# Kernel tuning notes

Hardware: AMD Instinct MI355X
Metric: run time of the kernel (lower is better)

The kernel has to match this reference:

```python
import jax, jax.numpy as jnp
import numpy as np

N = 50000      # nodes
D = 64         # hidden
EMB = 16       # emb_dims
E = 800000     # edges = N * knn(16)
R2 = 0.3 ** 2  # r^2 at epoch 0
GW = 1.0       # grav_weight at epoch 0
EPS = 1e-5


def _lin_params(k, fi, fo):
    kw, kb = jax.random.split(k)
    W = jax.random.normal(kw, (fi, fo), jnp.float32) / np.sqrt(fi).astype(np.float32)
    b = jax.random.normal(kb, (fo,), jnp.float32) * 0.01
    return W, b


def setup_inputs() -> dict:
    key = jax.random.key(0)
    ks = jax.random.split(key, 16)
    inp = {}
    inp['hidden_features'] = jax.random.normal(ks[0], (N, D), jnp.float32)
    inp['edge_index'] = jax.random.randint(ks[1], (2, E), 0, N, jnp.int32)
    inp['current_epoch'] = 0
    # spatial network: (D+1)->D->D->EMB, each Linear + LayerNorm + ReLU
    for i, (fi, fo) in enumerate([(D + 1, D), (D, D), (D, EMB)]):
        W, b = _lin_params(ks[2 + i], fi, fo)
        inp[f'sW{i}'] = W
        inp[f'sb{i}'] = b
        inp[f'sg{i}'] = jnp.ones((fo,), jnp.float32)
        inp[f'sB{i}'] = jnp.zeros((fo,), jnp.float32)
    # feature network: 2*(D+1)->D->D, each Linear + LayerNorm + ReLU
    for i, (fi, fo) in enumerate([(2 * (D + 1), D), (D, D)]):
        W, b = _lin_params(ks[8 + i], fi, fo)
        inp[f'fW{i}'] = W
        inp[f'fb{i}'] = b
        inp[f'fg{i}'] = jnp.ones((fo,), jnp.float32)
        inp[f'fB{i}'] = jnp.zeros((fo,), jnp.float32)
    return inp


def _ln(x, g, b):
    m = jnp.mean(x, axis=-1, keepdims=True)
    v = jnp.mean((x - m) ** 2, axis=-1, keepdims=True)
    return (x - m) * jax.lax.rsqrt(v + EPS) * g + b


def _blk(x, W, b, g, B):
    return jax.nn.relu(_ln(x @ W + b, g, B))


def reference(hidden_features, edge_index, current_epoch,
              sW0, sb0, sg0, sB0, sW1, sb1, sg1, sB1, sW2, sb2, sg2, sB2,
              fW0, fb0, fg0, fB0, fW1, fb1, fg1, fB1):
    # append per-node mean channel: [N, D] -> [N, D+1]
    h = jnp.concatenate([hidden_features,
                         jnp.mean(hidden_features, axis=1, keepdims=True)], axis=-1)
    # spatial embedding [N, EMB]
    s = _blk(_blk(_blk(h, sW0, sb0, sg0, sB0), sW1, sb1, sg1, sB1), sW2, sb2, sg2, sB2)
    start = edge_index[0]
    end = edge_index[1]
    # gravitational edge weight: exp(-grav_weight * ||s_i - s_j||^2 / r^2)
    d = jnp.sum((s[start] - s[end]) ** 2, axis=-1)  # [E]
    w = jnp.exp(-GW * d / R2)                        # [E]
    # gather -> weight -> scatter_add aggregation
    agg = jax.ops.segment_sum(h[start] * w[:, None], end, num_segments=h.shape[0])
    cat = jnp.concatenate([agg, h], axis=-1)  # [N, 2*(D+1)]
    out = _blk(_blk(cat, fW0, fb0, fg0, fB0), fW1, fb1, fg1, fB1)  # [N, D]
    return out, s
```

## Files before the change

kernel.cpp:

```cpp
#include <hip/hip_runtime.h>
#include <hip/hip_bf16.h>

#define NN 50000
#define DD 64
#define EMBD 16
#define EE 800000
#define CAP 64
#define TILES ((NN + 63) / 64)
#define AGGB ((NN + 3) / 4)

#define OW_S0 0
#define OW_S1 6656
#define OW_S2 11264
#define OW_F0 12416
#define OW_F1 23168
#define NWB   27776

typedef short s16x8 __attribute__((ext_vector_type(8)));
typedef float f32x4 __attribute__((ext_vector_type(4)));
typedef unsigned short ushort_t;

__device__ __forceinline__ float bcast(float v, int l) {
  return __int_as_float(__builtin_amdgcn_readlane(__float_as_int(v), l));
}

__device__ __forceinline__ unsigned short f2b(float x) {
  unsigned u = __float_as_uint(x);
  return (unsigned short)((u + 0x7FFFu + ((u >> 16) & 1u)) >> 16);
}

__device__ __forceinline__ float b2f(unsigned short u) {
  return __uint_as_float(((unsigned)u) << 16);
}

__device__ __forceinline__ float wred64f(float v) {
  v += __shfl_xor(v, 1);  v += __shfl_xor(v, 2);  v += __shfl_xor(v, 4);
  v += __shfl_xor(v, 8);  v += __shfl_xor(v, 16); v += __shfl_xor(v, 32);
  return v;
}

__global__ __launch_bounds__(256)
void GravConv3556_prep_k(const float* __restrict__ sW0, const float* __restrict__ sW1,
                         const float* __restrict__ sW2, const float* __restrict__ fW0,
                         const float* __restrict__ fW1, unsigned short* __restrict__ wb,
                         int* __restrict__ cnt)
{
  int i0 = blockIdx.x * 256 + threadIdx.x;
  int st = gridDim.x * 256;
  for (int i = i0; i < NN; i += st) cnt[i] = 0;
  for (int i = i0; i < 64 * 104; i += st) {
    int n = i / 104, k = i % 104;
    wb[OW_S0 + i] = (k < 65) ? f2b(sW0[k * 64 + n]) : (unsigned short)0;
  }
  for (int i = i0; i < 64 * 72; i += st) {
    int n = i / 72, k = i % 72;
    wb[OW_S1 + i] = (k < 64) ? f2b(sW1[k * 64 + n]) : (unsigned short)0;
  }
  for (int i = i0; i < 16 * 72; i += st) {
    int n = i / 72, k = i % 72;
    wb[OW_S2 + i] = (k < 64) ? f2b(sW2[k * 16 + n]) : (unsigned short)0;
  }
  for (int i = i0; i < 64 * 168; i += st) {
    int n = i / 168, k = i % 168;
    wb[OW_F0 + i] = (k < 130) ? f2b(fW0[k * 64 + n]) : (unsigned short)0;
  }
  for (int i = i0; i < 64 * 72; i += st) {
    int n = i / 72, k = i % 72;
    wb[OW_F1 + i] = (k < 64) ? f2b(fW1[k * 64 + n]) : (unsigned short)0;
  }
}

#define XROW 104
__global__ __launch_bounds__(256)
void GravConv3556_spatial_k(const float* __restrict__ hidden,
    const unsigned short* __restrict__ wb,
    const float* __restrict__ sb0, const float* __restrict__ sg0, const float* __restrict__ sB0,
    const float* __restrict__ sb1, const float* __restrict__ sg1, const float* __restrict__ sB1,
    const float* __restrict__ sb2, const float* __restrict__ sg2, const float* __restrict__ sB2,
    float* __restrict__ s_out)
{
  __shared__ unsigned short X[64 * XROW];
  __shared__ unsigned short W0[64 * XROW];
  __shared__ unsigned short W1[64 * 72];
  __shared__ unsigned short W2[16 * 72];
  int tid = threadIdx.x;
  int lane = tid & 63;
  int wv = tid >> 6;
  int c = lane & 15;
  int q = lane >> 4;
  int base = blockIdx.x * 64;

  {
    const uint4* g = (const uint4*)(wb + OW_S0); uint4* l = (uint4*)W0;
    for (int i = tid; i < 832; i += 256) l[i] = g[i];
    g = (const uint4*)(wb + OW_S1); l = (uint4*)W1;
    for (int i = tid; i < 576; i += 256) l[i] = g[i];
    g = (const uint4*)(wb + OW_S2); l = (uint4*)W2;
    for (int i = tid; i < 144; i += 256) l[i] = g[i];
  }
  for (int i = 0; i < 16; i++) {
    int m = wv * 16 + i;
    int node = base + m; if (node >= NN) node = NN - 1;
    float x = hidden[(size_t)node * 64 + lane];
    float mean = wred64f(x) * (1.0f / 64.0f);
    X[m * XROW + lane] = f2b(x);
    if (lane == 0) X[m * XROW + 64] = f2b(mean);
    if (lane < 39) X[m * XROW + 65 + lane] = 0;
  }
  __syncthreads();

  int mrow = wv * 16 + c;
  float z[16];

  {
    s16x8 a[3];
    #pragma unroll
    for (int kc = 0; kc < 3; kc++)
      a[kc] = *(const s16x8*)(X + mrow * XROW + kc * 32 + q * 8);
    #pragma unroll
    for (int nt = 0; nt < 4; nt++) {
      f32x4 acc = {0.f, 0.f, 0.f, 0.f};
      #pragma unroll
      for (int kc = 0; kc < 3; kc++) {
        s16x8 b = *(const s16x8*)(W0 + (nt * 16 + c) * XROW + kc * 32 + q * 8);
        acc = __builtin_amdgcn_mfma_f32_16x16x32_bf16(a[kc], b, acc, 0, 0, 0);
      }
      float bias = sb0[nt * 16 + c];
      #pragma unroll
      for (int reg = 0; reg < 4; reg++) z[nt * 4 + reg] = acc[reg] + bias;
    }
    #pragma unroll
    for (int reg = 0; reg < 4; reg++) {
      float s1 = z[reg] + z[4 + reg] + z[8 + reg] + z[12 + reg];
      float s2 = z[reg] * z[reg] + z[4 + reg] * z[4 + reg]
               + z[8 + reg] * z[8 + reg] + z[12 + reg] * z[12 + reg];
      s1 += __shfl_xor(s1, 1); s2 += __shfl_xor(s2, 1);
      s1 += __shfl_xor(s1, 2); s2 += __shfl_xor(s2, 2);
      s1 += __shfl_xor(s1, 4); s2 += __shfl_xor(s2, 4);
      s1 += __shfl_xor(s1, 8); s2 += __shfl_xor(s2, 8);
      float mu = s1 * (1.0f / 64.0f);
      float rs = rsqrtf(fmaxf(s2 * (1.0f / 64.0f) - mu * mu, 0.f) + 1e-5f);
      int m = wv * 16 + q * 4 + reg;
      #pragma unroll
      for (int nt = 0; nt < 4; nt++) {
        int n = nt * 16 + c;
        float y = fmaxf(fmaf((z[nt * 4 + reg] - mu) * rs, sg0[n], sB0[n]), 0.f);
        X[m * XROW + n] = f2b(y);
      }
    }
  }

  {
    s16x8 a[2];
    #pragma unroll
    for (int kc = 0; kc < 2; kc++)
      a[kc] = *(const s16x8*)(X + mrow * XROW + kc * 32 + q * 8);
    #pragma unroll
    for (int nt = 0; nt < 4; nt++) {
      f32x4 acc = {0.f, 0.f, 0.f, 0.f};
      #pragma unroll
      for (int kc = 0; kc < 2; kc++) {
        s16x8 b = *(const s16x8*)(W1 + (nt * 16 + c) * 72 + kc * 32 + q * 8);
        acc = __builtin_amdgcn_mfma_f32_16x16x32_bf16(a[kc], b, acc, 0, 0, 0);
      }
      float bias = sb1[nt * 16 + c];
      #pragma unroll
      for (int reg = 0; reg < 4; reg++) z[nt * 4 + reg] = acc[reg] + bias;
    }
    #pragma unroll
    for (int reg = 0; reg < 4; reg++) {
      float s1 = z[reg] + z[4 + reg] + z[8 + reg] + z[12 + reg];
      float s2 = z[reg] * z[reg] + z[4 + reg] * z[4 + reg]
               + z[8 + reg] * z[8 + reg] + z[12 + reg] * z[12 + reg];
      s1 += __shfl_xor(s1, 1); s2 += __shfl_xor(s2, 1);
      s1 += __shfl_xor(s1, 2); s2 += __shfl_xor(s2, 2);
      s1 += __shfl_xor(s1, 4); s2 += __shfl_xor(s2, 4);
      s1 += __shfl_xor(s1, 8); s2 += __shfl_xor(s2, 8);
      float mu = s1 * (1.0f / 64.0f);
      float rs = rsqrtf(fmaxf(s2 * (1.0f / 64.0f) - mu * mu, 0.f) + 1e-5f);
      int m = wv * 16 + q * 4 + reg;
      #pragma unroll
      for (int nt = 0; nt < 4; nt++) {
        int n = nt * 16 + c;
        float y = fmaxf(fmaf((z[nt * 4 + reg] - mu) * rs, sg1[n], sB1[n]), 0.f);
        X[m * XROW + n] = f2b(y);
      }
    }
  }

  {
    s16x8 a[2];
    #pragma unroll
    for (int kc = 0; kc < 2; kc++)
      a[kc] = *(const s16x8*)(X + mrow * XROW + kc * 32 + q * 8);
    f32x4 acc = {0.f, 0.f, 0.f, 0.f};
    #pragma unroll
    for (int kc = 0; kc < 2; kc++) {
      s16x8 b = *(const s16x8*)(W2 + c * 72 + kc * 32 + q * 8);
      acc = __builtin_amdgcn_mfma_f32_16x16x32_bf16(a[kc], b, acc, 0, 0, 0);
    }
    float bias = sb2[c];
    float z4[4];
    #pragma unroll
    for (int reg = 0; reg < 4; reg++) z4[reg] = acc[reg] + bias;
    #pragma unroll
    for (int reg = 0; reg < 4; reg++) {
      float s1 = z4[reg], s2 = z4[reg] * z4[reg];
      s1 += __shfl_xor(s1, 1); s2 += __shfl_xor(s2, 1);
      s1 += __shfl_xor(s1, 2); s2 += __shfl_xor(s2, 2);
      s1 += __shfl_xor(s1, 4); s2 += __shfl_xor(s2, 4);
      s1 += __shfl_xor(s1, 8); s2 += __shfl_xor(s2, 8);
      float mu = s1 * (1.0f / 16.0f);
      float rs = rsqrtf(fmaxf(s2 * (1.0f / 16.0f) - mu * mu, 0.f) + 1e-5f);
      float y = fmaxf(fmaf((z4[reg] - mu) * rs, sg2[c], sB2[c]), 0.f);
      int node = base + wv * 16 + q * 4 + reg;
      if (node < NN) s_out[(size_t)node * 16 + c] = y;
    }
  }
}

__global__ __launch_bounds__(256)
void GravConv3556_scatter_k(const int* __restrict__ ei, const float* __restrict__ s,
                            int* __restrict__ cnt, int2* __restrict__ pairs)
{
  int e = blockIdx.x * 256 + threadIdx.x;
  if (e >= EE) return;
  int a = ei[e];
  int b = ei[EE + e];
  const float4* sa = (const float4*)(s + (size_t)a * 16);
  const float4* sb = (const float4*)(s + (size_t)b * 16);
  float4 p0 = sa[0], p1 = sa[1], p2 = sa[2], p3 = sa[3];
  float4 q0 = sb[0], q1 = sb[1], q2 = sb[2], q3 = sb[3];
  float d = 0.f;
  d = fmaf(p0.x - q0.x, p0.x - q0.x, d); d = fmaf(p0.y - q0.y, p0.y - q0.y, d);
  d = fmaf(p0.z - q0.z, p0.z - q0.z, d); d = fmaf(p0.w - q0.w, p0.w - q0.w, d);
  d = fmaf(p1.x - q1.x, p1.x - q1.x, d); d = fmaf(p1.y - q1.y, p1.y - q1.y, d);
  d = fmaf(p1.z - q1.z, p1.z - q1.z, d); d = fmaf(p1.w - q1.w, p1.w - q1.w, d);
  d = fmaf(p2.x - q2.x, p2.x - q2.x, d); d = fmaf(p2.y - q2.y, p2.y - q2.y, d);
  d = fmaf(p2.z - q2.z, p2.z - q2.z, d); d = fmaf(p2.w - q2.w, p2.w - q2.w, d);
  d = fmaf(p3.x - q3.x, p3.x - q3.x, d); d = fmaf(p3.y - q3.y, p3.y - q3.y, d);
  d = fmaf(p3.z - q3.z, p3.z - q3.z, d); d = fmaf(p3.w - q3.w, p3.w - q3.w, d);
  float w = __expf(d * (-1.0f / 0.09f));
  int pos = atomicAdd(&cnt[b], 1);
  if (pos < CAP) pairs[(size_t)b * CAP + pos] = make_int2(a, __float_as_int(w));
}

__global__ __launch_bounds__(256)
void GravConv3556_agg_k(const float* __restrict__ hidden,
                        const int* __restrict__ cnt, const int2* __restrict__ pairs,
                        unsigned short* __restrict__ aggr)
{
  int lane = threadIdx.x & 63;
  int n = blockIdx.x * 4 + (threadIdx.x >> 6);
  if (n >= NN) return;
  int m = cnt[n]; if (m > CAP) m = CAP;
  float xa0 = 0.f, xa1 = 0.f, xa2 = 0.f, xa3 = 0.f;
  int2 pr = make_int2(0, 0);
  if (lane < m) pr = pairs[(size_t)n * CAP + lane];
  int aj = pr.x; float wj = __int_as_float(pr.y);
#define GSTEP(q, ACC) { int jj = jb + (q); int jc = jj < m ? jj : m - 1;        \
    int   a_ = __builtin_amdgcn_readlane(aj, jc);                               \
    float w_ = (jj < m) ? bcast(wj, jc) : 0.0f;                                 \
    ACC = fmaf(w_, hidden[(size_t)a_ * 64 + lane], ACC); }
  for (int jb = 0; jb < m; jb += 8) {
    GSTEP(0, xa0) GSTEP(1, xa1) GSTEP(2, xa2) GSTEP(3, xa3)
    GSTEP(4, xa0) GSTEP(5, xa1) GSTEP(6, xa2) GSTEP(7, xa3)
  }
#undef GSTEP
  aggr[(size_t)n * 64 + lane] = f2b((xa0 + xa1) + (xa2 + xa3));
}

#define CROW 168
__global__ __launch_bounds__(256)
void GravConv3556_feature_k(const float* __restrict__ hidden,
    const unsigned short* __restrict__ aggr, const unsigned short* __restrict__ wb,
    const float* __restrict__ fb0, const float* __restrict__ fg0, const float* __restrict__ fB0,
    const float* __restrict__ fb1, const float* __restrict__ fg1, const float* __restrict__ fB1,
    float* __restrict__ out)
{
  __shared__ unsigned short catB[64 * CROW];
  __shared__ unsigned short W0T[64 * CROW];
  __shared__ unsigned short W1T[64 * 72];
  int tid = threadIdx.x;
  int lane = tid & 63;
  int wv = tid >> 6;
  int c = lane & 15;
  int q = lane >> 4;
  int base = blockIdx.x * 64;

  {
    const uint4* g = (const uint4*)(wb + OW_F0); uint4* l = (uint4*)W0T;
    for (int i = tid; i < 1344; i += 256) l[i] = g[i];
    g = (const uint4*)(wb + OW_F1); l = (uint4*)W1T;
    for (int i = tid; i < 576; i += 256) l[i] = g[i];
  }

  for (int i = 0; i < 16; i++) {
    int m = wv * 16 + i;
    int node = base + m; if (node >= NN) node = NN - 1;
    unsigned short ra = aggr[(size_t)node * 64 + lane];
    float xa = b2f(ra);
    float mA = wred64f(xa) * (1.0f / 64.0f);
    catB[m * CROW + lane] = ra;
    float xh = hidden[(size_t)node * 64 + lane];
    float mB = wred64f(xh) * (1.0f / 64.0f);
    catB[m * CROW + 65 + lane] = f2b(xh);
    if (lane == 0) {
      catB[m * CROW + 64] = f2b(mA);
      catB[m * CROW + 129] = f2b(mB);
    }
    if (lane < 38) catB[m * CROW + 130 + lane] = 0;
  }
  __syncthreads();

  int mrow = wv * 16 + c;

  s16x8 a0[5];
  #pragma unroll
  for (int kc = 0; kc < 5; kc++)
    a0[kc] = *(const s16x8*)(catB + mrow * CROW + kc * 32 + q * 8);

  float z[16];
  #pragma unroll
  for (int nt = 0; nt < 4; nt++) {
    f32x4 acc = {0.f, 0.f, 0.f, 0.f};
    #pragma unroll
    for (int kc = 0; kc < 5; kc++) {
      s16x8 b = *(const s16x8*)(W0T + (nt * 16 + c) * CROW + kc * 32 + q * 8);
      acc = __builtin_amdgcn_mfma_f32_16x16x32_bf16(a0[kc], b, acc, 0, 0, 0);
    }
    float bias = fb0[nt * 16 + c];
    #pragma unroll
    for (int reg = 0; reg < 4; reg++) z[nt * 4 + reg] = acc[reg] + bias;
  }
  #pragma unroll
  for (int reg = 0; reg < 4; reg++) {
    float s1 = z[reg] + z[4 + reg] + z[8 + reg] + z[12 + reg];
    float s2 = z[reg] * z[reg] + z[4 + reg] * z[4 + reg]
             + z[8 + reg] * z[8 + reg] + z[12 + reg] * z[12 + reg];
    s1 += __shfl_xor(s1, 1); s2 += __shfl_xor(s2, 1);
    s1 += __shfl_xor(s1, 2); s2 += __shfl_xor(s2, 2);
    s1 += __shfl_xor(s1, 4); s2 += __shfl_xor(s2, 4);
    s1 += __shfl_xor(s1, 8); s2 += __shfl_xor(s2, 8);
    float mu = s1 * (1.0f / 64.0f);
    float rs = rsqrtf(fmaxf(s2 * (1.0f / 64.0f) - mu * mu, 0.f) + 1e-5f);
    int m = wv * 16 + q * 4 + reg;
    #pragma unroll
    for (int nt = 0; nt < 4; nt++) {
      int n = nt * 16 + c;
      float y = fmaxf(fmaf((z[nt * 4 + reg] - mu) * rs, fg0[n], fB0[n]), 0.f);
      catB[m * CROW + n] = f2b(y);
    }
  }

  s16x8 a1[2];
  #pragma unroll
  for (int kc = 0; kc < 2; kc++)
    a1[kc] = *(const s16x8*)(catB + mrow * CROW + kc * 32 + q * 8);

  #pragma unroll
  for (int nt = 0; nt < 4; nt++) {
    f32x4 acc = {0.f, 0.f, 0.f, 0.f};
    #pragma unroll
    for (int kc = 0; kc < 2; kc++) {
      s16x8 b = *(const s16x8*)(W1T + (nt * 16 + c) * 72 + kc * 32 + q * 8);
      acc = __builtin_amdgcn_mfma_f32_16x16x32_bf16(a1[kc], b, acc, 0, 0, 0);
    }
    float bias = fb1[nt * 16 + c];
    #pragma unroll
    for (int reg = 0; reg < 4; reg++) z[nt * 4 + reg] = acc[reg] + bias;
  }
  #pragma unroll
  for (int reg = 0; reg < 4; reg++) {
    float s1 = z[reg] + z[4 + reg] + z[8 + reg] + z[12 + reg];
    float s2 = z[reg] * z[reg] + z[4 + reg] * z[4 + reg]
             + z[8 + reg] * z[8 + reg] + z[12 + reg] * z[12 + reg];
    s1 += __shfl_xor(s1, 1); s2 += __shfl_xor(s2, 1);
    s1 += __shfl_xor(s1, 2); s2 += __shfl_xor(s2, 2);
    s1 += __shfl_xor(s1, 4); s2 += __shfl_xor(s2, 4);
    s1 += __shfl_xor(s1, 8); s2 += __shfl_xor(s2, 8);
    float mu = s1 * (1.0f / 64.0f);
    float rs = rsqrtf(fmaxf(s2 * (1.0f / 64.0f) - mu * mu, 0.f) + 1e-5f);
    int node = base + wv * 16 + q * 4 + reg;
    if (node < NN) {
      #pragma unroll
      for (int nt = 0; nt < 4; nt++) {
        int n = nt * 16 + c;
        float y = fmaxf(fmaf((z[nt * 4 + reg] - mu) * rs, fg1[n], fB1[n]), 0.f);
        out[(size_t)node * 64 + n] = y;
      }
    }
  }
}

extern "C" void kernel_launch(void* const* d_in, const int* in_sizes, int n_in,
                              void* d_out, int out_size, void* d_ws, size_t ws_size,
                              hipStream_t stream) {
  const float* hidden = (const float*)d_in[0];
  const int*   ei     = (const int*)d_in[1];
  const float *sW0 = (const float*)d_in[3],  *sb0 = (const float*)d_in[4],
              *sg0 = (const float*)d_in[5],  *sB0 = (const float*)d_in[6];
  const float *sW1 = (const float*)d_in[7],  *sb1 = (const float*)d_in[8],
              *sg1 = (const float*)d_in[9],  *sB1 = (const float*)d_in[10];
  const float *sW2 = (const float*)d_in[11], *sb2 = (const float*)d_in[12],
              *sg2 = (const float*)d_in[13], *sB2 = (const float*)d_in[14];
  const float *fW0 = (const float*)d_in[15], *fb0 = (const float*)d_in[16],
              *fg0 = (const float*)d_in[17], *fB0 = (const float*)d_in[18];
  const float *fW1 = (const float*)d_in[19], *fb1 = (const float*)d_in[20],
              *fg1 = (const float*)d_in[21], *fB1 = (const float*)d_in[22];

  float* out   = (float*)d_out;
  float* s_out = out + (size_t)NN * 64;

  int2*  pairs = (int2*)d_ws;
  int*   cnt   = (int*)(pairs + (size_t)NN * CAP);
  unsigned short* aggr = (unsigned short*)(cnt + NN);
  unsigned short* wbuf =
      (unsigned short*)(((uintptr_t)(aggr + (size_t)NN * 64) + 15) & ~(uintptr_t)15);

  GravConv3556_prep_k<<<32, 256, 0, stream>>>(sW0, sW1, sW2, fW0, fW1, wbuf, cnt);
  GravConv3556_spatial_k<<<TILES, 256, 0, stream>>>(hidden, wbuf,
      sb0, sg0, sB0, sb1, sg1, sB1, sb2, sg2, sB2, s_out);
  GravConv3556_scatter_k<<<(EE + 255) / 256, 256, 0, stream>>>(ei, s_out, cnt, pairs);
  GravConv3556_agg_k<<<AGGB, 256, 0, stream>>>(hidden, cnt, pairs, aggr);
  GravConv3556_feature_k<<<TILES, 256, 0, stream>>>(hidden, aggr, wbuf,
      fb0, fg0, fB0, fb1, fg1, fB1, out);
}
```

Before: 241.7 us.

## Partition scatter/agg by XCD and gather fp16 copies of hidden and embeddings

The scatter kernel now launches 8×64 blocks, where each block owns one eighth of the destination nodes (mapped to an XCD via blockIdx&7) and scans a chunk of edges, skipping edges whose destination lies outside its range. The aggregation kernel uses the same XCD-to-node mapping, so cnt, pairs and the gathered rows stay in one XCD's L2. The hidden features and spatial embeddings are also converted to fp16 copies (in prep and spatial), halving the bytes of the random gathers, and CAP drops to 48 to shrink the pairs buffer. In exchange, every block reads each edge destination index eight times overall, fp16 adds precision loss, and any node with more than 48 incoming edges is truncated, which could drop edges from random graphs.

```diff
diff --git a/kernel.cpp b/kernel.cpp
--- a/kernel.cpp
+++ b/kernel.cpp
@@ -1,13 +1,18 @@
 #include <hip/hip_runtime.h>
 #include <hip/hip_bf16.h>
+#include <hip/hip_fp16.h>
 
 #define NN 50000
 #define DD 64
 #define EMBD 16
 #define EE 800000
-#define CAP 64
+#define CAP 48
+#define NXCD 8
+#define XNODES (NN / NXCD)
+#define SCHUNKS 64
+#define SCE (EE / SCHUNKS)
 #define TILES ((NN + 63) / 64)
-#define AGGB ((NN + 3) / 4)
+#define AGGB (NXCD * ((XNODES + 3) / 4))
 
 #define OW_S0 0
 #define OW_S1 6656
@@ -18,7 +23,7 @@
 
 typedef short s16x8 __attribute__((ext_vector_type(8)));
 typedef float f32x4 __attribute__((ext_vector_type(4)));
-typedef unsigned short ushort_t;
+typedef _Float16 h16x8 __attribute__((ext_vector_type(8)));
 
 __device__ __forceinline__ float bcast(float v, int l) {
   return __int_as_float(__builtin_amdgcn_readlane(__float_as_int(v), l));
@@ -31,6 +36,10 @@
 
 __device__ __forceinline__ float b2f(unsigned short u) {
   return __uint_as_float(((unsigned)u) << 16);
+}
+
+__device__ __forceinline__ unsigned short f2h(float x) {
+  return __half_as_ushort(__float2half(x));
 }
 
 __device__ __forceinline__ float wred64f(float v) {
@@ -42,12 +51,23 @@
 __global__ __launch_bounds__(256)
 void GravConv3556_prep_k(const float* __restrict__ sW0, const float* __restrict__ sW1,
                          const float* __restrict__ sW2, const float* __restrict__ fW0,
-                         const float* __restrict__ fW1, unsigned short* __restrict__ wb,
+                         const float* __restrict__ fW1, const float* __restrict__ hidden,
+                         unsigned short* __restrict__ wb, unsigned short* __restrict__ hid16,
                          int* __restrict__ cnt)
 {
   int i0 = blockIdx.x * 256 + threadIdx.x;
   int st = gridDim.x * 256;
   for (int i = i0; i < NN; i += st) cnt[i] = 0;
+  {
+    const float4* hf = (const float4*)hidden;
+    ushort4* hh = (ushort4*)hid16;
+    for (int i = i0; i < NN * 16; i += st) {
+      float4 v = hf[i];
+      ushort4 o;
+      o.x = f2h(v.x); o.y = f2h(v.y); o.z = f2h(v.z); o.w = f2h(v.w);
+      hh[i] = o;
+    }
+  }
   for (int i = i0; i < 64 * 104; i += st) {
     int n = i / 104, k = i % 104;
     wb[OW_S0 + i] = (k < 65) ? f2b(sW0[k * 64 + n]) : (unsigned short)0;
@@ -77,7 +97,7 @@
     const float* __restrict__ sb0, const float* __restrict__ sg0, const float* __restrict__ sB0,
     const float* __restrict__ sb1, const float* __restrict__ sg1, const float* __restrict__ sB1,
     const float* __restrict__ sb2, const float* __restrict__ sg2, const float* __restrict__ sB2,
-    float* __restrict__ s_out)
+    float* __restrict__ s_out, unsigned short* __restrict__ s16)
 {
   __shared__ unsigned short X[64 * XROW];
   __shared__ unsigned short W0[64 * XROW];
@@ -214,45 +234,59 @@
       float rs = rsqrtf(fmaxf(s2 * (1.0f / 16.0f) - mu * mu, 0.f) + 1e-5f);
       float y = fmaxf(fmaf((z4[reg] - mu) * rs, sg2[c], sB2[c]), 0.f);
       int node = base + wv * 16 + q * 4 + reg;
-      if (node < NN) s_out[(size_t)node * 16 + c] = y;
+      if (node < NN) {
+        s_out[(size_t)node * 16 + c] = y;
+        s16[(size_t)node * 16 + c] = f2h(y);
+      }
     }
   }
 }
 
 __global__ __launch_bounds__(256)
-void GravConv3556_scatter_k(const int* __restrict__ ei, const float* __restrict__ s,
+void GravConv3556_scatter_k(const int* __restrict__ ei, const unsigned short* __restrict__ s16,
                             int* __restrict__ cnt, int2* __restrict__ pairs)
 {
-  int e = blockIdx.x * 256 + threadIdx.x;
-  if (e >= EE) return;
-  int a = ei[e];
-  int b = ei[EE + e];
-  const float4* sa = (const float4*)(s + (size_t)a * 16);
-  const float4* sb = (const float4*)(s + (size_t)b * 16);
-  float4 p0 = sa[0], p1 = sa[1], p2 = sa[2], p3 = sa[3];
-  float4 q0 = sb[0], q1 = sb[1], q2 = sb[2], q3 = sb[3];
-  float d = 0.f;
-  d = fmaf(p0.x - q0.x, p0.x - q0.x, d); d = fmaf(p0.y - q0.y, p0.y - q0.y, d);
-  d = fmaf(p0.z - q0.z, p0.z - q0.z, d); d = fmaf(p0.w - q0.w, p0.w - q0.w, d);
-  d = fmaf(p1.x - q1.x, p1.x - q1.x, d); d = fmaf(p1.y - q1.y, p1.y - q1.y, d);
-  d = fmaf(p1.z - q1.z, p1.z - q1.z, d); d = fmaf(p1.w - q1.w, p1.w - q1.w, d);
-  d = fmaf(p2.x - q2.x, p2.x - q2.x, d); d = fmaf(p2.y - q2.y, p2.y - q2.y, d);
-  d = fmaf(p2.z - q2.z, p2.z - q2.z, d); d = fmaf(p2.w - q2.w, p2.w - q2.w, d);
-  d = fmaf(p3.x - q3.x, p3.x - q3.x, d); d = fmaf(p3.y - q3.y, p3.y - q3.y, d);
-  d = fmaf(p3.z - q3.z, p3.z - q3.z, d); d = fmaf(p3.w - q3.w, p3.w - q3.w, d);
-  float w = __expf(d * (-1.0f / 0.09f));
-  int pos = atomicAdd(&cnt[b], 1);
-  if (pos < CAP) pairs[(size_t)b * CAP + pos] = make_int2(a, __float_as_int(w));
+  int xcd = blockIdx.x & 7;
+  int chunk = blockIdx.x >> 3;
+  int lo = xcd * XNODES;
+  int e0 = chunk * SCE;
+  int e1 = e0 + SCE;
+  const _Float16* s = (const _Float16*)s16;
+  for (int e = e0 + threadIdx.x; e < e1; e += 256) {
+    int b = ei[EE + e];
+    unsigned rb = (unsigned)(b - lo);
+    if (rb >= (unsigned)XNODES) continue;
+    int a = ei[e];
+    const h16x8* sa = (const h16x8*)(s + (size_t)a * 16);
+    const h16x8* sb = (const h16x8*)(s + (size_t)b * 16);
+    h16x8 p0 = sa[0], p1 = sa[1];
+    h16x8 q0 = sb[0], q1 = sb[1];
+    float d = 0.f;
+    #pragma unroll
+    for (int t = 0; t < 8; t++) {
+      float u = (float)p0[t] - (float)q0[t];
+      d = fmaf(u, u, d);
+      float v = (float)p1[t] - (float)q1[t];
+      d = fmaf(v, v, d);
+    }
+    float w = __expf(d * (-1.0f / 0.09f));
+    int pos = atomicAdd(&cnt[b], 1);
+    if (pos < CAP) pairs[(size_t)b * CAP + pos] = make_int2(a, __float_as_int(w));
+  }
 }
 
 __global__ __launch_bounds__(256)
-void GravConv3556_agg_k(const float* __restrict__ hidden,
+void GravConv3556_agg_k(const unsigned short* __restrict__ hid16,
                         const int* __restrict__ cnt, const int2* __restrict__ pairs,
                         unsigned short* __restrict__ aggr)
 {
   int lane = threadIdx.x & 63;
-  int n = blockIdx.x * 4 + (threadIdx.x >> 6);
-  if (n >= NN) return;
+  int xcd = blockIdx.x & 7;
+  int j = blockIdx.x >> 3;
+  int rn = j * 4 + (threadIdx.x >> 6);
+  if (rn >= XNODES) return;
+  int n = xcd * XNODES + rn;
+  const _Float16* hid = (const _Float16*)hid16;
   int m = cnt[n]; if (m > CAP) m = CAP;
   float xa0 = 0.f, xa1 = 0.f, xa2 = 0.f, xa3 = 0.f;
   int2 pr = make_int2(0, 0);
@@ -261,7 +295,7 @@
 #define GSTEP(q, ACC) { int jj = jb + (q); int jc = jj < m ? jj : m - 1;        \
     int   a_ = __builtin_amdgcn_readlane(aj, jc);                               \
     float w_ = (jj < m) ? bcast(wj, jc) : 0.0f;                                 \
-    ACC = fmaf(w_, hidden[(size_t)a_ * 64 + lane], ACC); }
+    ACC = fmaf(w_, (float)hid[(size_t)a_ * 64 + lane], ACC); }
   for (int jb = 0; jb < m; jb += 8) {
     GSTEP(0, xa0) GSTEP(1, xa1) GSTEP(2, xa2) GSTEP(3, xa3)
     GSTEP(4, xa0) GSTEP(5, xa1) GSTEP(6, xa2) GSTEP(7, xa3)
@@ -414,15 +448,17 @@
 
   int2*  pairs = (int2*)d_ws;
   int*   cnt   = (int*)(pairs + (size_t)NN * CAP);
-  unsigned short* aggr = (unsigned short*)(cnt + NN);
-  unsigned short* wbuf =
-      (unsigned short*)(((uintptr_t)(aggr + (size_t)NN * 64) + 15) & ~(uintptr_t)15);
-
-  GravConv3556_prep_k<<<32, 256, 0, stream>>>(sW0, sW1, sW2, fW0, fW1, wbuf, cnt);
+  unsigned short* aggr  = (unsigned short*)(cnt + NN);
+  unsigned short* hid16 = aggr + (size_t)NN * 64;
+  unsigned short* s16   = hid16 + (size_t)NN * 64;
+  unsigned short* wbuf  = s16 + (size_t)NN * 16;
+
+  GravConv3556_prep_k<<<200, 256, 0, stream>>>(sW0, sW1, sW2, fW0, fW1, hidden,
+                                               wbuf, hid16, cnt);
   GravConv3556_spatial_k<<<TILES, 256, 0, stream>>>(hidden, wbuf,
-      sb0, sg0, sB0, sb1, sg1, sB1, sb2, sg2, sB2, s_out);
-  GravConv3556_scatter_k<<<(EE + 255) / 256, 256, 0, stream>>>(ei, s_out, cnt, pairs);
-  GravConv3556_agg_k<<<AGGB, 256, 0, stream>>>(hidden, cnt, pairs, aggr);
+      sb0, sg0, sB0, sb1, sg1, sB1, sb2, sg2, sB2, s_out, s16);
+  GravConv3556_scatter_k<<<NXCD * SCHUNKS, 256, 0, stream>>>(ei, s16, cnt, pairs);
+  GravConv3556_agg_k<<<AGGB, 256, 0, stream>>>(hid16, cnt, pairs, aggr);
   GravConv3556_feature_k<<<TILES, 256, 0, stream>>>(hidden, aggr, wbuf,
       fb0, fg0, fB0, fb1, fg1, fB1, out);
 }
```

Measured after the change: 263.7 us. +9.1%, slower.
